# Kernel optimization log

Measured on AMD Instinct MI355X. Metric: run time of the kernel, lower is better.

Reference implementation:

```python
import jax, jax.numpy as jnp
import numpy as np

B, S, E = 8, 4096, 1024
H, W = 8, 128          # num_heads, window_size
D = E // H             # head_dim = 128


def setup_inputs() -> dict:
    key = jax.random.key(0)
    ks = jax.random.split(key, 8)
    values = jax.random.normal(ks[0], (B, S, E), dtype=jnp.float32)
    keys = jax.random.normal(ks[1], (B, S, E), dtype=jnp.float32)
    query = jax.random.normal(ks[2], (B, S, E), dtype=jnp.float32)
    # per-head projections: nn.Linear(head_dim, head_dim, bias=False), W shape [out,in]
    Wv = jax.random.normal(ks[3], (D, D), dtype=jnp.float32) * 0.02
    Wk = jax.random.normal(ks[4], (D, D), dtype=jnp.float32) * 0.02
    Wq = jax.random.normal(ks[5], (D, D), dtype=jnp.float32) * 0.02
    # fc_out: nn.Linear(E, E) with bias
    Wo = jax.random.normal(ks[6], (E, E), dtype=jnp.float32) * 0.02
    bo = jax.random.normal(ks[7], (E,), dtype=jnp.float32) * 0.02
    return {"values": values, "keys": keys, "query": query,
            "Wv": Wv, "Wk": Wk, "Wq": Wq, "Wo": Wo, "bo": bo}


def _local_attention(q, k, v, w):
    # q,k,v: [B,H,S,D]; non-causal sliding window: look_backward=1, look_forward=1
    b, h, s, d = q.shape
    n = s // w  # number of windows
    scale = d ** -0.5
    qw = q.reshape(b, h, n, w, d)
    kw = k.reshape(b, h, n, w, d)
    vw = v.reshape(b, h, n, w, d)
    # look-around gather: for window i, keys from windows [i-1, i, i+1]
    kpad = jnp.pad(kw, ((0, 0), (0, 0), (1, 1), (0, 0), (0, 0)))
    vpad = jnp.pad(vw, ((0, 0), (0, 0), (1, 1), (0, 0), (0, 0)))
    kg = jnp.concatenate([kpad[:, :, i:i + n] for i in range(3)], axis=3)  # [B,H,n,3w,D]
    vg = jnp.concatenate([vpad[:, :, i:i + n] for i in range(3)], axis=3)
    sim = jnp.einsum('bhnqd,bhnkd->bhnqk', qw * scale, kg)  # [B,H,n,w,3w]
    # mask out-of-range (padded) neighbor windows at the sequence boundaries
    valid = jnp.ones((n, 3 * w), dtype=bool)
    valid = valid.at[0, :w].set(False)        # first window has no look-backward
    valid = valid.at[n - 1, 2 * w:].set(False)  # last window has no look-forward
    sim = jnp.where(valid[None, None, :, None, :], sim, jnp.finfo(sim.dtype).min)
    attn = jax.nn.softmax(sim, axis=-1)
    out = jnp.einsum('bhnqk,bhnkd->bhnqd', attn, vg)
    return out.reshape(b, h, s, d)


def reference(values, keys, query, Wv, Wk, Wq, Wo, bo):
    b, s, _ = query.shape
    # reshape to heads, apply per-head linear (x @ W.T), move heads to dim 1
    vr = values.reshape(b, s, H, D)
    kr = keys.reshape(b, s, H, D)
    qr = query.reshape(b, s, H, D)
    v = jnp.einsum('bshd,od->bhso', vr, Wv)
    k = jnp.einsum('bshd,od->bhso', kr, Wk)
    q = jnp.einsum('bshd,od->bhso', qr, Wq)
    out = _local_attention(q, k, v, W)            # [B,H,S,D]
    out = out.transpose(0, 2, 1, 3).reshape(b, s, H * D)
    return jnp.einsum('bse,oe->bso', out, Wo) + bo
```

## Files before the change

### kernel.cpp

```cpp
#include <hip/hip_runtime.h>


typedef __attribute__((ext_vector_type(8))) short short8;
typedef __attribute__((ext_vector_type(4))) short short4v;
typedef __attribute__((ext_vector_type(4))) float float4v;

#define MFMA16(a, b, c) __builtin_amdgcn_mfma_f32_16x16x32_bf16((a), (b), (c), 0, 0, 0)

constexpr int NW_ = 32;
constexpr int LD_ = 136;

__device__ __forceinline__ unsigned short f2bf(float f) {
  unsigned u = __builtin_bit_cast(unsigned, f);
  u += 0x7fffu + ((u >> 16) & 1u);
  return (unsigned short)(u >> 16);
}

__device__ __forceinline__ short8 pack8(float4v a0, float4v a1) {
  short8 s;
  for (int j = 0; j < 4; ++j) { s[j] = (short)f2bf(a0[j]); s[4 + j] = (short)f2bf(a1[j]); }
  return s;
}

__device__ __forceinline__ void gload16(const unsigned short* g, unsigned short* l) {
  __builtin_amdgcn_global_load_lds(
      (const __attribute__((address_space(1))) unsigned int*)g,
      (__attribute__((address_space(3))) unsigned int*)l, 16, 0, 0);
}

__global__ __launch_bounds__(256) void proj_kernel(
    const float* __restrict__ x, const float* __restrict__ w,
    unsigned short* __restrict__ out) {
  __shared__ unsigned short lA[128 * LD_];
  __shared__ unsigned short lB[128 * LD_];
  const int tid = threadIdx.x;
  const long m0 = (long)blockIdx.x * 128;

  for (int idx = tid; idx < 2048; idx += 256) {
    const float* src = x + m0 * 128 + (long)idx * 8;
    float4v a0 = *(const float4v*)(src);
    float4v a1 = *(const float4v*)(src + 4);
    *(short8*)&lA[(idx >> 4) * LD_ + (idx & 15) * 8] = pack8(a0, a1);
  }
  for (int idx = tid; idx < 2048; idx += 256) {
    const float* src = w + idx * 8;
    float4v a0 = *(const float4v*)(src);
    float4v a1 = *(const float4v*)(src + 4);
    *(short8*)&lB[(idx >> 4) * LD_ + (idx & 15) * 8] = pack8(a0, a1);
  }
  __syncthreads();

  const int wv = tid >> 6, L = tid & 63, lr = L & 15, lg = L >> 4;
  const int wm = wv >> 1, wn = wv & 1;
  float4v acc[4][4];
  for (int a = 0; a < 4; ++a)
    for (int b = 0; b < 4; ++b)
      for (int r = 0; r < 4; ++r) acc[a][b][r] = 0.f;

  for (int ks = 0; ks < 4; ++ks) {
    short8 af[4], bf[4];
    for (int mt = 0; mt < 4; ++mt)
      af[mt] = *(const short8*)&lA[(wm * 64 + mt * 16 + lr) * LD_ + ks * 32 + lg * 8];
    for (int nt = 0; nt < 4; ++nt)
      bf[nt] = *(const short8*)&lB[(wn * 64 + nt * 16 + lr) * LD_ + ks * 32 + lg * 8];
    for (int mt = 0; mt < 4; ++mt)
      for (int nt = 0; nt < 4; ++nt)
        acc[mt][nt] = MFMA16(af[mt], bf[nt], acc[mt][nt]);
  }
  __syncthreads();
  for (int mt = 0; mt < 4; ++mt)
    for (int nt = 0; nt < 4; ++nt)
      for (int r = 0; r < 4; ++r)
        lA[(wm * 64 + mt * 16 + lg * 4 + r) * LD_ + wn * 64 + nt * 16 + lr] =
            f2bf(acc[mt][nt][r]);
  __syncthreads();
  for (int idx = tid; idx < 2048; idx += 256) {
    int r = idx >> 4, c = idx & 15;
    long row = m0 + r;
    int b = (int)(row >> 15), s = (int)((row >> 3) & 4095), h = (int)(row & 7);
    long g = ((long)(b * 8 + h) * 4096 + s) * 128 + c * 8;
    *(short8*)(out + g) = *(const short8*)&lA[r * LD_ + c * 8];
  }
}

__global__ __launch_bounds__(512, 2) void attn_kernel(
    const unsigned short* __restrict__ qp, const unsigned short* __restrict__ kp,
    const unsigned short* __restrict__ vp, unsigned short* __restrict__ op) {
  __shared__ unsigned short lQ[128 * LD_];
  __shared__ unsigned short lK[128 * LD_];
  __shared__ unsigned short lV[128 * LD_];
  const int tid = threadIdx.x;
  const int bid = blockIdx.x;
  const int b = bid >> 8, h = (bid >> 5) & 7, i = bid & 31;
  const long base = (long)(b * 8 + h) * (4096L * 128);

  for (int idx = tid; idx < 2048; idx += 512)
    *(short8*)&lQ[(idx >> 4) * LD_ + (idx & 15) * 8] =
        *(const short8*)(qp + base + (long)i * 16384 + (long)idx * 8);

  const int wv = tid >> 6, L = tid & 63, lr = L & 15, lg = L >> 4;
  const bool valid[3] = {i > 0, true, i < NW_ - 1};
  float4v Sacc[3][8];

  for (int j = 0; j < 3; ++j) {
    if (!valid[j]) continue;
    const int jw = i - 1 + j;
    __syncthreads();
    for (int idx = tid; idx < 2048; idx += 512)
      *(short8*)&lK[(idx >> 4) * LD_ + (idx & 15) * 8] =
          *(const short8*)(kp + base + (long)jw * 16384 + (long)idx * 8);
    __syncthreads();
    for (int mt = 0; mt < 8; ++mt)
      for (int r = 0; r < 4; ++r) Sacc[j][mt][r] = 0.f;
    for (int ks = 0; ks < 4; ++ks) {
      short8 bq = *(const short8*)&lQ[(wv * 16 + lr) * LD_ + ks * 32 + lg * 8];
      for (int mt = 0; mt < 8; ++mt) {
        short8 ak = *(const short8*)&lK[(mt * 16 + lr) * LD_ + ks * 32 + lg * 8];
        Sacc[j][mt] = MFMA16(ak, bq, Sacc[j][mt]);
      }
    }
  }

  float mraw = -3.0e38f;
  for (int j = 0; j < 3; ++j) {
    if (!valid[j]) continue;
    for (int mt = 0; mt < 8; ++mt)
      for (int r = 0; r < 4; ++r) mraw = fmaxf(mraw, Sacc[j][mt][r]);
  }
  mraw = fmaxf(mraw, __shfl_xor(mraw, 16));
  mraw = fmaxf(mraw, __shfl_xor(mraw, 32));
  const float csc = 0.08838834764831845f * 1.4426950408889634f;
  const float mm = mraw * csc;
  float lsum = 0.f;
  float4v Oacc[8];
  for (int mt = 0; mt < 8; ++mt)
    for (int r = 0; r < 4; ++r) Oacc[mt][r] = 0.f;

  for (int j = 0; j < 3; ++j) {
    if (!valid[j]) continue;
    const int jw = i - 1 + j;
    __syncthreads();
    for (int mt = 0; mt < 8; ++mt) {
      short4v pk;
      for (int r = 0; r < 4; ++r) {
        float p = exp2f(Sacc[j][mt][r] * csc - mm);
        lsum += p;
        pk[r] = (short)f2bf(p);
      }
      *(short4v*)&lK[(wv * 16 + lr) * LD_ + mt * 16 + lg * 4] = pk;
    }
    for (int idx = tid; idx < 1024; idx += 512) {
      int pr = idx & 63, c = idx >> 6;
      const unsigned short* src = vp + base + (long)jw * 16384 + (long)(2 * pr) * 128 + c * 8;
      short8 v0 = *(const short8*)(src);
      short8 v1 = *(const short8*)(src + 128);
      for (int jj = 0; jj < 8; ++jj) {
        unsigned val = ((unsigned)(unsigned short)v0[jj]) |
                       (((unsigned)(unsigned short)v1[jj]) << 16);
        *(unsigned*)&lV[(c * 8 + jj) * LD_ + 2 * pr] = val;
      }
    }
    __syncthreads();
    for (int ks = 0; ks < 4; ++ks) {
      short8 bp = *(const short8*)&lK[(wv * 16 + lr) * LD_ + ks * 32 + lg * 8];
      for (int mt = 0; mt < 8; ++mt) {
        short8 av = *(const short8*)&lV[(mt * 16 + lr) * LD_ + ks * 32 + lg * 8];
        Oacc[mt] = MFMA16(av, bp, Oacc[mt]);
      }
    }
  }

  lsum += __shfl_xor(lsum, 16);
  lsum += __shfl_xor(lsum, 32);
  const float rl = 1.f / lsum;
  const long obase = base + (long)i * 16384;
  for (int mt = 0; mt < 8; ++mt) {
    short4v ok;
    for (int r = 0; r < 4; ++r) ok[r] = (short)f2bf(Oacc[mt][r] * rl);
    *(short4v*)(op + obase + (long)(wv * 16 + lr) * 128 + mt * 16 + lg * 4) = ok;
  }
}

__global__ __launch_bounds__(256) void cvt_wo(
    const float* __restrict__ w, unsigned short* __restrict__ o) {
  long idx = (long)blockIdx.x * 256 + threadIdx.x;
  const float* src = w + idx * 8;
  float4v a0 = *(const float4v*)(src);
  float4v a1 = *(const float4v*)(src + 4);
  *(short8*)(o + idx * 8) = pack8(a0, a1);
}

__global__ __launch_bounds__(256) void outproj_kernel(
    const unsigned short* __restrict__ O, const unsigned short* __restrict__ Wob,
    const float* __restrict__ bo, float* __restrict__ out) {
  __shared__ unsigned short lA[128 * 64];
  __shared__ unsigned short lB[128 * 64];
  const int tid = threadIdx.x;
  const long m0 = (long)blockIdx.x * 128;
  const int n0 = blockIdx.y * 128;
  const int wv = tid >> 6, L = tid & 63, lr = L & 15, lg = L >> 4;
  const int wm = wv >> 1, wn = wv & 1;

  const int rsub = L >> 3;
  const int xg = ((L & 7) ^ rsub) * 8;

  const int bb = (int)(m0 >> 12);
  const int sbase = (int)(m0 & 4095);
  long Abase[4], Bbase[4];
#pragma unroll
  for (int t = 0; t < 4; ++t) {
    int r = wv * 32 + t * 8 + rsub;
    Abase[t] = (long)bb * 4194304 + (long)(sbase + r) * 128 + xg;
    Bbase[t] = (long)(n0 + r) * 1024 + xg;
  }

  float4v acc[4][4];
  for (int a = 0; a < 4; ++a)
    for (int b = 0; b < 4; ++b)
      for (int r = 0; r < 4; ++r) acc[a][b][r] = 0.f;

  for (int kk = 0; kk < 1024; kk += 64) {
    const long aoff = ((long)(kk >> 7) << 19) + (kk & 64);
    __syncthreads();
#pragma unroll
    for (int t = 0; t < 4; ++t) {
      gload16(O + Abase[t] + aoff, &lA[(wv * 32 + t * 8) * 64]);
      gload16(Wob + Bbase[t] + kk, &lB[(wv * 32 + t * 8) * 64]);
    }
    __syncthreads();
#pragma unroll
    for (int ks = 0; ks < 2; ++ks) {
      short8 af[4], bw[4];
      const int gsw = ((ks * 4 + lg) ^ (lr & 7)) << 3;
#pragma unroll
      for (int mt = 0; mt < 4; ++mt)
        af[mt] = *(const short8*)&lA[(wm * 64 + mt * 16 + lr) * 64 + gsw];
#pragma unroll
      for (int nt = 0; nt < 4; ++nt)
        bw[nt] = *(const short8*)&lB[(wn * 64 + nt * 16 + lr) * 64 + gsw];
#pragma unroll
      for (int mt = 0; mt < 4; ++mt)
#pragma unroll
        for (int nt = 0; nt < 4; ++nt)
          acc[mt][nt] = MFMA16(af[mt], bw[nt], acc[mt][nt]);
    }
  }

  for (int nt = 0; nt < 4; ++nt) {
    float bv = bo[n0 + wn * 64 + nt * 16 + lr];
    for (int mt = 0; mt < 4; ++mt)
      for (int r = 0; r < 4; ++r)
        out[(m0 + wm * 64 + mt * 16 + lg * 4 + r) * 1024 + n0 + wn * 64 + nt * 16 + lr] =
            acc[mt][nt][r] + bv;
  }
}

extern "C" void kernel_launch(void* const* d_in, const int* in_sizes, int n_in,
                              void* d_out, int out_size, void* d_ws, size_t ws_size,
                              hipStream_t stream) {
  const float* values = (const float*)d_in[0];
  const float* keys   = (const float*)d_in[1];
  const float* query  = (const float*)d_in[2];
  const float* Wv     = (const float*)d_in[3];
  const float* Wk     = (const float*)d_in[4];
  const float* Wq     = (const float*)d_in[5];
  const float* Wo     = (const float*)d_in[6];
  const float* bo     = (const float*)d_in[7];
  float* out = (float*)d_out;

  const size_t plane = 8UL * 8 * 4096 * 128;
  unsigned short* qp = (unsigned short*)d_ws;
  unsigned short* kp = qp + plane;
  unsigned short* vp = kp + plane;

  proj_kernel<<<2048, 256, 0, stream>>>(query, Wq, qp);
  proj_kernel<<<2048, 256, 0, stream>>>(keys, Wk, kp);
  proj_kernel<<<2048, 256, 0, stream>>>(values, Wv, vp);
  attn_kernel<<<2048, 512, 0, stream>>>(qp, kp, vp, qp);
  cvt_wo<<<512, 256, 0, stream>>>(Wo, kp);
  outproj_kernel<<<dim3(256, 8), 256, 0, stream>>>(qp, kp, bo, out);
}
```

Baseline: 753.7 us.

## Restructure local attention into online-softmax loop over 64-key chunks with double-buffered K

The attention kernel now streams keys in 64-row chunks and uses an online softmax (running max and rescale) instead of holding all three windows' scores in registers. K chunks are double-buffered in LDS via async loads with an XOR swizzle, and Q is kept in registers. P is passed to the PV MFMA through lane shuffles instead of an LDS round trip, and V is transposed into a swizzled LDS layout. LDS and register use drop so occupancy can rise to 4 blocks per CU, and block IDs are remapped. In exchange the loop runs more iterations, adds rescaling arithmetic and cross-lane shuffles, and the swizzle indexing is intricate and easy to get wrong.

```diff
diff --git a/kernel.cpp b/kernel.cpp
--- a/kernel.cpp
+++ b/kernel.cpp
@@ -4,6 +4,7 @@
 typedef __attribute__((ext_vector_type(8))) short short8;
 typedef __attribute__((ext_vector_type(4))) short short4v;
 typedef __attribute__((ext_vector_type(4))) float float4v;
+typedef __attribute__((ext_vector_type(4))) unsigned int uint4v;
 
 #define MFMA16(a, b, c) __builtin_amdgcn_mfma_f32_16x16x32_bf16((a), (b), (c), 0, 0, 0)
 
@@ -83,88 +84,137 @@
   }
 }
 
-__global__ __launch_bounds__(512, 2) void attn_kernel(
+__global__ __launch_bounds__(512, 4) void attn_kernel(
     const unsigned short* __restrict__ qp, const unsigned short* __restrict__ kp,
     const unsigned short* __restrict__ vp, unsigned short* __restrict__ op) {
-  __shared__ unsigned short lQ[128 * LD_];
-  __shared__ unsigned short lK[128 * LD_];
-  __shared__ unsigned short lV[128 * LD_];
+  __shared__ unsigned short lK[2][64 * 128];
+  __shared__ unsigned short lV[128 * 64];
   const int tid = threadIdx.x;
-  const int bid = blockIdx.x;
+  const int bid0 = blockIdx.x;
+  const int bid = (bid0 & 7) * 256 + (bid0 >> 3);
   const int b = bid >> 8, h = (bid >> 5) & 7, i = bid & 31;
   const long base = (long)(b * 8 + h) * (4096L * 128);
 
-  for (int idx = tid; idx < 2048; idx += 512)
-    *(short8*)&lQ[(idx >> 4) * LD_ + (idx & 15) * 8] =
-        *(const short8*)(qp + base + (long)i * 16384 + (long)idx * 8);
-
   const int wv = tid >> 6, L = tid & 63, lr = L & 15, lg = L >> 4;
-  const bool valid[3] = {i > 0, true, i < NW_ - 1};
-  float4v Sacc[3][8];
-
-  for (int j = 0; j < 3; ++j) {
-    if (!valid[j]) continue;
-    const int jw = i - 1 + j;
-    __syncthreads();
-    for (int idx = tid; idx < 2048; idx += 512)
-      *(short8*)&lK[(idx >> 4) * LD_ + (idx & 15) * 8] =
-          *(const short8*)(kp + base + (long)jw * 16384 + (long)idx * 8);
-    __syncthreads();
-    for (int mt = 0; mt < 8; ++mt)
-      for (int r = 0; r < 4; ++r) Sacc[j][mt][r] = 0.f;
-    for (int ks = 0; ks < 4; ++ks) {
-      short8 bq = *(const short8*)&lQ[(wv * 16 + lr) * LD_ + ks * 32 + lg * 8];
-      for (int mt = 0; mt < 8; ++mt) {
-        short8 ak = *(const short8*)&lK[(mt * 16 + lr) * LD_ + ks * 32 + lg * 8];
-        Sacc[j][mt] = MFMA16(ak, bq, Sacc[j][mt]);
-      }
-    }
-  }
-
-  float mraw = -3.0e38f;
-  for (int j = 0; j < 3; ++j) {
-    if (!valid[j]) continue;
-    for (int mt = 0; mt < 8; ++mt)
-      for (int r = 0; r < 4; ++r) mraw = fmaxf(mraw, Sacc[j][mt][r]);
-  }
-  mraw = fmaxf(mraw, __shfl_xor(mraw, 16));
-  mraw = fmaxf(mraw, __shfl_xor(mraw, 32));
+  const int rsub = L >> 4;
+  const int gsrc = (L & 15) ^ rsub;
+
+  const int kc0 = (i > 0) ? 2 * i - 2 : 0;
+  const int kc1 = (i < NW_ - 1) ? 2 * i + 4 : 2 * i + 2;
+
+  const unsigned short* qrow = qp + base + (long)i * 16384 + (long)(wv * 16 + lr) * 128;
+  short8 bq[4];
+#pragma unroll
+  for (int ks = 0; ks < 4; ++ks) bq[ks] = *(const short8*)(qrow + ks * 32 + lg * 8);
+
+  {
+    const unsigned short* ksrc = kp + base + (long)kc0 * 8192;
+#pragma unroll
+    for (int t = 0; t < 2; ++t)
+      gload16(ksrc + (long)(wv * 8 + t * 4 + rsub) * 128 + ((gsrc ^ (t << 2)) << 3),
+              &lK[0][(wv * 8 + t * 4) * 128]);
+  }
+
   const float csc = 0.08838834764831845f * 1.4426950408889634f;
-  const float mm = mraw * csc;
-  float lsum = 0.f;
+  float mm = -3.0e38f, lsum = 0.f;
   float4v Oacc[8];
+#pragma unroll
   for (int mt = 0; mt < 8; ++mt)
     for (int r = 0; r < 4; ++r) Oacc[mt][r] = 0.f;
 
-  for (int j = 0; j < 3; ++j) {
-    if (!valid[j]) continue;
-    const int jw = i - 1 + j;
+  int cur = 0;
+  for (int c = kc0; c < kc1; ++c, cur ^= 1) {
     __syncthreads();
-    for (int mt = 0; mt < 8; ++mt) {
-      short4v pk;
-      for (int r = 0; r < 4; ++r) {
-        float p = exp2f(Sacc[j][mt][r] * csc - mm);
-        lsum += p;
-        pk[r] = (short)f2bf(p);
+
+    if (c + 1 < kc1) {
+      const unsigned short* ksrc = kp + base + (long)(c + 1) * 8192;
+#pragma unroll
+      for (int t = 0; t < 2; ++t)
+        gload16(ksrc + (long)(wv * 8 + t * 4 + rsub) * 128 + ((gsrc ^ (t << 2)) << 3),
+                &lK[cur ^ 1][(wv * 8 + t * 4) * 128]);
+    }
+
+    const unsigned short* vsrc = vp + base + (long)c * 8192 +
+                                 (long)(2 * (L & 31)) * 128 + wv * 16 + ((L >> 5) << 3);
+    short8 va = *(const short8*)(vsrc);
+    short8 vb = *(const short8*)(vsrc + 128);
+
+    float4v Sacc[4];
+#pragma unroll
+    for (int mt = 0; mt < 4; ++mt)
+      for (int r = 0; r < 4; ++r) Sacc[mt][r] = 0.f;
+#pragma unroll
+    for (int ks = 0; ks < 4; ++ks) {
+#pragma unroll
+      for (int mt = 0; mt < 4; ++mt) {
+        short8 ak = *(const short8*)&lK[cur][(mt * 16 + lr) * 128 +
+                                            ((((ks << 2) + lg) ^ (lr & 7)) << 3)];
+        Sacc[mt] = MFMA16(ak, bq[ks], Sacc[mt]);
       }
-      *(short4v*)&lK[(wv * 16 + lr) * LD_ + mt * 16 + lg * 4] = pk;
-    }
-    for (int idx = tid; idx < 1024; idx += 512) {
-      int pr = idx & 63, c = idx >> 6;
-      const unsigned short* src = vp + base + (long)jw * 16384 + (long)(2 * pr) * 128 + c * 8;
-      short8 v0 = *(const short8*)(src);
-      short8 v1 = *(const short8*)(src + 128);
+    }
+
+    float cmax = -3.0e38f;
+#pragma unroll
+    for (int mt = 0; mt < 4; ++mt)
+      for (int r = 0; r < 4; ++r) cmax = fmaxf(cmax, Sacc[mt][r]);
+    cmax = fmaxf(cmax, __shfl_xor(cmax, 16));
+    cmax = fmaxf(cmax, __shfl_xor(cmax, 32));
+    const float mmN = fmaxf(mm, cmax * csc);
+    const float f = exp2f(mm - mmN);
+    mm = mmN;
+    lsum *= f;
+#pragma unroll
+    for (int mt = 0; mt < 8; ++mt)
+      for (int r = 0; r < 4; ++r) Oacc[mt][r] *= f;
+
+    unsigned pk2[8];
+#pragma unroll
+    for (int mt = 0; mt < 4; ++mt) {
+      float p0 = exp2f(Sacc[mt][0] * csc - mmN);
+      float p1 = exp2f(Sacc[mt][1] * csc - mmN);
+      float p2 = exp2f(Sacc[mt][2] * csc - mmN);
+      float p3 = exp2f(Sacc[mt][3] * csc - mmN);
+      lsum += (p0 + p1) + (p2 + p3);
+      pk2[2 * mt]     = (unsigned)f2bf(p0) | ((unsigned)f2bf(p1) << 16);
+      pk2[2 * mt + 1] = (unsigned)f2bf(p2) | ((unsigned)f2bf(p3) << 16);
+    }
+
+    {
+      const int p = L & 31;
+      const int dbase = wv * 16 + ((L >> 5) << 3);
+#pragma unroll
       for (int jj = 0; jj < 8; ++jj) {
-        unsigned val = ((unsigned)(unsigned short)v0[jj]) |
-                       (((unsigned)(unsigned short)v1[jj]) << 16);
-        *(unsigned*)&lV[(c * 8 + jj) * LD_ + 2 * pr] = val;
+        unsigned val = ((unsigned)(unsigned short)va[jj]) |
+                       (((unsigned)(unsigned short)vb[jj]) << 16);
+        *(unsigned*)((char*)lV + (dbase + jj) * 128 +
+                     ((((p >> 2) ^ jj) << 4) | ((p & 3) << 2))) = val;
       }
     }
+
     __syncthreads();
-    for (int ks = 0; ks < 4; ++ks) {
-      short8 bp = *(const short8*)&lK[(wv * 16 + lr) * LD_ + ks * 32 + lg * 8];
+
+    const int sel = (lg >> 1) & 1;
+    const int srcA = ((lg & 1) << 5) + lr;
+#pragma unroll
+    for (int ks = 0; ks < 2; ++ks) {
+      unsigned u0A = __shfl(pk2[4 * ks + 0], srcA);
+      unsigned u1A = __shfl(pk2[4 * ks + 1], srcA);
+      unsigned w0A = __shfl(pk2[4 * ks + 2], srcA);
+      unsigned w1A = __shfl(pk2[4 * ks + 3], srcA);
+      unsigned u0B = __shfl(pk2[4 * ks + 0], srcA + 16);
+      unsigned u1B = __shfl(pk2[4 * ks + 1], srcA + 16);
+      unsigned w0B = __shfl(pk2[4 * ks + 2], srcA + 16);
+      unsigned w1B = __shfl(pk2[4 * ks + 3], srcA + 16);
+      uint4v t;
+      t[0] = sel ? w0A : u0A;
+      t[1] = sel ? w1A : u1A;
+      t[2] = sel ? w0B : u0B;
+      t[3] = sel ? w1B : u1B;
+      short8 bp = __builtin_bit_cast(short8, t);
+#pragma unroll
       for (int mt = 0; mt < 8; ++mt) {
-        short8 av = *(const short8*)&lV[(mt * 16 + lr) * LD_ + ks * 32 + lg * 8];
+        short8 av = *(const short8*)&lV[(mt * 16 + lr) * 64 +
+                                        ((((ks << 2) + lg) ^ (lr & 7)) << 3)];
         Oacc[mt] = MFMA16(av, bp, Oacc[mt]);
       }
     }
@@ -174,6 +224,7 @@
   lsum += __shfl_xor(lsum, 32);
   const float rl = 1.f / lsum;
   const long obase = base + (long)i * 16384;
+#pragma unroll
   for (int mt = 0; mt < 8; ++mt) {
     short4v ok;
     for (int r = 0; r < 4; ++r) ok[r] = (short)f2bf(Oacc[mt][r] * rl);
```

Measured after the change: 685.1 us. -9.1%, faster.
